# Kernel tuning notes

Hardware: AMD Instinct MI355X
Metric: run time of the kernel (lower is better)

Reference implementation:

```python
import jax, jax.numpy as jnp
import numpy as np
import math

L_S = 64  # segment length (factor)


def setup_inputs() -> dict:
    key = jax.random.key(0)
    kq, kk, kv = jax.random.split(key, 3)
    B, L, H, D = 4, 8192, 16, 64
    return {
        "queries": jax.random.normal(kq, (B, L, H, D), dtype=jnp.float32),
        "keys": jax.random.normal(kk, (B, L, H, D), dtype=jnp.float32),
        "values": jax.random.normal(kv, (B, L, H, D), dtype=jnp.float32),
        "attn_mask": 0,
    }


def reference(queries, keys, values, attn_mask):
    B, L, H, D = queries.shape
    Ls = L_S
    M = L // Ls  # L % Ls == 0 by construction, so addition_Q path is a no-op
    scale = 1.0 / math.sqrt(Ls * D)

    # segment: [B, M, Ls, H, D]
    sq = queries.reshape(B, M, Ls, H, D)
    sk = keys.reshape(B, M, Ls, H, D)
    sv = values.reshape(B, M, Ls, H, D)

    # rfft over head dim D, ortho norm -> [B, M, Ls, H, D//2+1] complex
    qf = jnp.fft.rfft(sq, axis=-1, norm="ortho")
    kf = jnp.fft.rfft(sk, axis=-1, norm="ortho")
    vf = jnp.fft.rfft(sv, axis=-1, norm="ortho")

    # complex segment correlation: [B, H, M, M]
    scores = jnp.einsum("bmlhd,bnlhd->bhmn", qf, jnp.conj(kf)) / math.sqrt(D)
    A = jax.nn.softmax(scale * jnp.abs(scores), axis=-1)  # real
    Ac = A.astype(qf.dtype)  # complex with zero imaginary part

    # complex weighted sum of value spectra: [B, M, Ls, H, D//2+1]
    Vf = jnp.einsum("bhmn,bnlhd->bmlhd", Ac, vf)
    V = jnp.fft.irfft(Vf, n=D, axis=-1, norm="ortho")  # real [B, M, Ls, H, D]
    return V.reshape(B, L, H, D)
```

## Files before the change

### kernel.cpp

```cpp
#include <hip/hip_runtime.h>
#include <cstdint>
#include <cstddef>


typedef short bf16x8 __attribute__((ext_vector_type(8)));
typedef float f32x4 __attribute__((ext_vector_type(4)));

__device__ __forceinline__ ushort f2bf(float f) {
    union { float f; uint32_t u; } v; v.f = f;
    uint32_t r = (v.u + 0x7FFFu + ((v.u >> 16) & 1u)) >> 16;
    return (ushort)r;
}

__global__ void k_gmat(float* __restrict__ GreT, float* __restrict__ GimT) {
    const float lam = 1.0f / 32768.0f;
    const float c = 3.14159265358979323846f / 32.0f;
    for (int e = threadIdx.x + blockIdx.x * blockDim.x; e < 4096; e += blockDim.x * gridDim.x) {
        int dp = e >> 6, d = e & 63;
        int delta = d - dp;
        float re = 0.f, im = 0.f;
        for (int k = 0; k <= 32; ++k) {
            int r = ((k * delta) % 64 + 64) % 64;
            float ang = c * (float)r;
            re += cosf(ang);
            im -= sinf(ang);
        }
        GreT[e] = re * lam;
        GimT[e] = im * lam;
    }
}

__global__ __launch_bounds__(256) void k_prep_q(const float* __restrict__ Q, ushort* __restrict__ Qf) {
    int blk = blockIdx.x;
    int bh = blk >> 7, m = blk & 127;
    int b = bh >> 4, h = bh & 15;
    const float* qbase = Q + ((size_t)(b * 8192 + m * 64)) * 1024 + h * 64;
    ushort* obase = Qf + ((size_t)bh * 128 + m) * 4096;
    for (int idx = threadIdx.x; idx < 1024; idx += 256) {
        int l = idx >> 4, d4 = (idx & 15) * 4;
        float4 v = *(const float4*)(qbase + (size_t)l * 1024 + d4);
        ushort4 o; o.x = f2bf(v.x); o.y = f2bf(v.y); o.z = f2bf(v.z); o.w = f2bf(v.w);
        *(ushort4*)(obase + idx * 4) = o;
    }
}

__global__ __launch_bounds__(256) void k_prep_k(const float* __restrict__ K,
                                                const float* __restrict__ GreT,
                                                const float* __restrict__ GimT,
                                                ushort* __restrict__ Kre, ushort* __restrict__ Kim) {
    __shared__ float gre[4096], gim[4096], kT[4096];
    int blk = blockIdx.x;
    int bh = blk >> 7, n = blk & 127;
    int b = bh >> 4, h = bh & 15;
    int t = threadIdx.x;
    for (int idx = t; idx < 1024; idx += 256) {
        *(float4*)&gre[idx * 4] = *(const float4*)(GreT + idx * 4);
        *(float4*)&gim[idx * 4] = *(const float4*)(GimT + idx * 4);
    }
    int lc = t & 63, dq = t >> 6;
    const float* kbase = K + ((size_t)(b * 8192 + n * 64 + lc)) * 1024 + h * 64;
    #pragma unroll
    for (int r = 0; r < 4; ++r) {
        int d0 = r * 16 + dq * 4;
        float4 v = *(const float4*)(kbase + d0);
        kT[(d0 + 0) * 64 + lc] = v.x; kT[(d0 + 1) * 64 + lc] = v.y;
        kT[(d0 + 2) * 64 + lc] = v.z; kT[(d0 + 3) * 64 + lc] = v.w;
    }
    __syncthreads();
    int d = t & 63, w = t >> 6;
    float re[16], im[16];
    #pragma unroll
    for (int j = 0; j < 16; ++j) { re[j] = 0.f; im[j] = 0.f; }
    for (int dp = 0; dp < 64; ++dp) {
        float gr = gre[dp * 64 + d];
        float gi = gim[dp * 64 + d];
        const float4* kp = (const float4*)&kT[dp * 64 + w * 16];
        #pragma unroll
        for (int q = 0; q < 4; ++q) {
            float4 kv = kp[q];
            re[q * 4 + 0] += gr * kv.x; re[q * 4 + 1] += gr * kv.y;
            re[q * 4 + 2] += gr * kv.z; re[q * 4 + 3] += gr * kv.w;
            im[q * 4 + 0] += gi * kv.x; im[q * 4 + 1] += gi * kv.y;
            im[q * 4 + 2] += gi * kv.z; im[q * 4 + 3] += gi * kv.w;
        }
    }
    ushort* reb = Kre + ((size_t)bh * 128 + n) * 4096;
    ushort* imb = Kim + ((size_t)bh * 128 + n) * 4096;
    #pragma unroll
    for (int j = 0; j < 16; ++j) {
        int off = (w * 16 + j) * 64 + d;
        reb[off] = f2bf(re[j]);
        imb[off] = f2bf(im[j]);
    }
}

__global__ __launch_bounds__(256) void k_scores(const ushort* __restrict__ Qf,
                                                const ushort* __restrict__ Kre,
                                                const ushort* __restrict__ Kim,
                                                float* __restrict__ Sre, float* __restrict__ Sim) {
    __shared__ ushort qt[64 * 72], ret[64 * 72], imt[64 * 72];
    int bh = blockIdx.y;
    int mh = blockIdx.x >> 1, nh = blockIdx.x & 1;
    int m0 = mh * 64, n0 = nh * 64;
    int t = threadIdx.x;
    int lane = t & 63, wave = t >> 6;
    int wm = wave >> 1, wn = wave & 1;
    int row16 = lane & 15, quad = lane >> 4;
    f32x4 accre[2][2] = {};
    f32x4 accim[2][2] = {};
    const ushort* qg = Qf + ((size_t)bh * 128 + m0) * 4096;
    const ushort* rg = Kre + ((size_t)bh * 128 + n0) * 4096;
    const ushort* ig = Kim + ((size_t)bh * 128 + n0) * 4096;
    for (int kt = 0; kt < 64; ++kt) {
        int j0 = kt * 64;
        #pragma unroll
        for (int p = 0; p < 2; ++p) {
            int idx = p * 256 + t;
            int row = idx >> 3, ch = idx & 7;
            size_t go = (size_t)row * 4096 + j0 + ch * 8;
            int lo = row * 72 + ch * 8;
            *(uint4*)&qt[lo]  = *(const uint4*)(qg + go);
            *(uint4*)&ret[lo] = *(const uint4*)(rg + go);
            *(uint4*)&imt[lo] = *(const uint4*)(ig + go);
        }
        __syncthreads();
        #pragma unroll
        for (int kk = 0; kk < 2; ++kk) {
            bf16x8 a[2], br[2], bi[2];
            #pragma unroll
            for (int mt = 0; mt < 2; ++mt)
                a[mt] = *(const bf16x8*)&qt[(wm * 32 + mt * 16 + row16) * 72 + kk * 32 + quad * 8];
            #pragma unroll
            for (int nt = 0; nt < 2; ++nt) {
                br[nt] = *(const bf16x8*)&ret[(wn * 32 + nt * 16 + row16) * 72 + kk * 32 + quad * 8];
                bi[nt] = *(const bf16x8*)&imt[(wn * 32 + nt * 16 + row16) * 72 + kk * 32 + quad * 8];
            }
            #pragma unroll
            for (int mt = 0; mt < 2; ++mt)
                #pragma unroll
                for (int nt = 0; nt < 2; ++nt) {
                    accre[mt][nt] = __builtin_amdgcn_mfma_f32_16x16x32_bf16(a[mt], br[nt], accre[mt][nt], 0, 0, 0);
                    accim[mt][nt] = __builtin_amdgcn_mfma_f32_16x16x32_bf16(a[mt], bi[nt], accim[mt][nt], 0, 0, 0);
                }
        }
        __syncthreads();
    }
    float* sre = Sre + (size_t)bh * 16384;
    float* sim = Sim + (size_t)bh * 16384;
    #pragma unroll
    for (int mt = 0; mt < 2; ++mt)
        #pragma unroll
        for (int nt = 0; nt < 2; ++nt)
            #pragma unroll
            for (int i = 0; i < 4; ++i) {
                int r = m0 + wm * 32 + mt * 16 + quad * 4 + i;
                int c = n0 + wn * 32 + nt * 16 + row16;
                sre[r * 128 + c] = accre[mt][nt][i];
                sim[r * 128 + c] = accim[mt][nt][i];
            }
}

__global__ __launch_bounds__(128) void k_softmax(const float* __restrict__ Sre,
                                                 const float* __restrict__ Sim,
                                                 ushort* __restrict__ A) {
    __shared__ float redmax[2], redsum[2];
    int row = blockIdx.x;
    int t = threadIdx.x;
    size_t off = (size_t)row * 128 + t;
    float re = Sre[off], im = Sim[off];
    float lg = sqrtf(re * re + im * im);
    float v = lg;
    for (int o = 32; o > 0; o >>= 1) v = fmaxf(v, __shfl_xor(v, o));
    if ((t & 63) == 0) redmax[t >> 6] = v;
    __syncthreads();
    float mx = fmaxf(redmax[0], redmax[1]);
    float e = expf(lg - mx);
    float s = e;
    for (int o = 32; o > 0; o >>= 1) s += __shfl_xor(s, o);
    if ((t & 63) == 0) redsum[t >> 6] = s;
    __syncthreads();
    float tot = redsum[0] + redsum[1];
    A[off] = f2bf(e / tot);
}

__global__ __launch_bounds__(256) void k_vt(const float* __restrict__ V, ushort* __restrict__ Vt) {
    __shared__ float tile[64 * 68];
    int l = blockIdx.x, nh = blockIdx.y, bh = blockIdx.z;
    int b = bh >> 4, h = bh & 15;
    int t = threadIdx.x;
    int n = t & 63, dq = t >> 6;
    const float* vbase = V + ((size_t)(b * 8192 + (nh * 64 + n) * 64 + l)) * 1024 + h * 64;
    #pragma unroll
    for (int r = 0; r < 4; ++r) {
        int d0 = r * 16 + dq * 4;
        float4 v = *(const float4*)(vbase + d0);
        tile[(d0 + 0) * 68 + n] = v.x; tile[(d0 + 1) * 68 + n] = v.y;
        tile[(d0 + 2) * 68 + n] = v.z; tile[(d0 + 3) * 68 + n] = v.w;
    }
    __syncthreads();
    int d = t >> 2, cq = t & 3;
    __align__(16) ushort u[16];
    #pragma unroll
    for (int i = 0; i < 16; ++i) u[i] = f2bf(tile[d * 68 + cq * 16 + i]);
    ushort* ob = Vt + ((size_t)bh * 4096 + l * 64 + d) * 128 + nh * 64 + cq * 16;
    *(uint4*)(ob) = *(uint4*)&u[0];
    *(uint4*)(ob + 8) = *(uint4*)&u[8];
}

__global__ __launch_bounds__(256) void k_mix(const ushort* __restrict__ A,
                                             const ushort* __restrict__ Vt,
                                             float* __restrict__ Out) {
    __shared__ ushort At[128 * 136], Vtl[64 * 136];
    int jt = blockIdx.x, bh = blockIdx.y;
    int b = bh >> 4, h = bh & 15;
    int j0 = jt * 64;
    int t = threadIdx.x;
    int lane = t & 63, wave = t >> 6;
    int row16 = lane & 15, quad = lane >> 4;
    const ushort* ag = A + (size_t)bh * 16384;
    const ushort* vg = Vt + ((size_t)bh * 4096 + j0) * 128;
    #pragma unroll
    for (int p = 0; p < 8; ++p) {
        int idx = p * 256 + t;
        int row = idx >> 4, ch = idx & 15;
        *(uint4*)&At[row * 136 + ch * 8] = *(const uint4*)(ag + row * 128 + ch * 8);
    }
    #pragma unroll
    for (int p = 0; p < 4; ++p) {
        int idx = p * 256 + t;
        int row = idx >> 4, ch = idx & 15;
        *(uint4*)&Vtl[row * 136 + ch * 8] = *(const uint4*)(vg + (size_t)row * 128 + ch * 8);
    }
    __syncthreads();
    f32x4 acc[2][4] = {};
    #pragma unroll
    for (int kk = 0; kk < 4; ++kk) {
        bf16x8 a[2], bv[4];
        #pragma unroll
        for (int mt = 0; mt < 2; ++mt)
            a[mt] = *(const bf16x8*)&At[(wave * 32 + mt * 16 + row16) * 136 + kk * 32 + quad * 8];
        #pragma unroll
        for (int j2 = 0; j2 < 4; ++j2)
            bv[j2] = *(const bf16x8*)&Vtl[(j2 * 16 + row16) * 136 + kk * 32 + quad * 8];
        #pragma unroll
        for (int mt = 0; mt < 2; ++mt)
            #pragma unroll
            for (int j2 = 0; j2 < 4; ++j2)
                acc[mt][j2] = __builtin_amdgcn_mfma_f32_16x16x32_bf16(a[mt], bv[j2], acc[mt][j2], 0, 0, 0);
    }
    #pragma unroll
    for (int mt = 0; mt < 2; ++mt)
        #pragma unroll
        for (int j2 = 0; j2 < 4; ++j2)
            #pragma unroll
            for (int i = 0; i < 4; ++i) {
                int m = wave * 32 + mt * 16 + quad * 4 + i;
                int j = j0 + j2 * 16 + row16;
                int ll = j >> 6, d = j & 63;
                Out[((size_t)(b * 8192 + m * 64 + ll)) * 1024 + h * 64 + d] = acc[mt][j2][i];
            }
}

extern "C" void kernel_launch(void* const* d_in, const int* in_sizes, int n_in,
                              void* d_out, int out_size, void* d_ws, size_t ws_size,
                              hipStream_t stream) {
    const float* Q = (const float*)d_in[0];
    const float* K = (const float*)d_in[1];
    const float* V = (const float*)d_in[2];
    float* Out = (float*)d_out;
    char* ws = (char*)d_ws;
    float* GreT = (float*)ws;
    float* GimT = (float*)(ws + 16384);
    float* Sre  = (float*)(ws + 32768);
    float* Sim  = (float*)(ws + 32768 + 4194304);
    ushort* A   = (ushort*)(ws + 32768 + 2 * 4194304);
    ushort* Qf  = (ushort*)(ws + 32768 + 2 * 4194304 + 2097152);
    ushort* Kre = Qf + 33554432;
    ushort* Kim = Kre + 33554432;
    ushort* Vt  = Qf;

    k_gmat<<<16, 256, 0, stream>>>(GreT, GimT);
    k_prep_q<<<8192, 256, 0, stream>>>(Q, Qf);
    k_prep_k<<<8192, 256, 0, stream>>>(K, GreT, GimT, Kre, Kim);
    k_scores<<<dim3(4, 64), 256, 0, stream>>>(Qf, Kre, Kim, Sre, Sim);
    k_softmax<<<8192, 128, 0, stream>>>(Sre, Sim, A);
    k_vt<<<dim3(64, 2, 64), 256, 0, stream>>>(V, Vt);
    k_mix<<<dim3(64, 64), 256, 0, stream>>>(A, Vt, Out);
}
```

Before: 613.8 us.

## Compute K spectral transform with bf16 MFMA using split hi/lo G matrices

The per-segment K transform (a 64x64 matrix times the 64x64 G matrix) moves from scalar fp32 FMAs in shared memory to bf16 MFMA instructions. G is stored as high and low bf16 parts, so two MFMAs per tile keep near-fp32 accuracy in the G operand, while K is rounded to bf16 before the multiply. G fragments are loaded straight from global memory into registers, and shared memory drops from 48KB to about 9KB, which should allow more blocks per CU. The cost is lower precision on the K input and output stores that are scattered by MFMA row layout.

```diff
diff --git a/kernel.cpp b/kernel.cpp
--- a/kernel.cpp
+++ b/kernel.cpp
@@ -12,11 +12,17 @@
     return (ushort)r;
 }
 
-__global__ void k_gmat(float* __restrict__ GreT, float* __restrict__ GimT) {
+__device__ __forceinline__ float bf2f(ushort h) {
+    union { uint32_t u; float f; } v; v.u = ((uint32_t)h) << 16;
+    return v.f;
+}
+
+__global__ void k_gmat(ushort* __restrict__ GreH, ushort* __restrict__ GreL,
+                       ushort* __restrict__ GimH, ushort* __restrict__ GimL) {
     const float lam = 1.0f / 32768.0f;
     const float c = 3.14159265358979323846f / 32.0f;
     for (int e = threadIdx.x + blockIdx.x * blockDim.x; e < 4096; e += blockDim.x * gridDim.x) {
-        int dp = e >> 6, d = e & 63;
+        int d = e >> 6, dp = e & 63;
         int delta = d - dp;
         float re = 0.f, im = 0.f;
         for (int k = 0; k <= 32; ++k) {
@@ -25,8 +31,13 @@
             re += cosf(ang);
             im -= sinf(ang);
         }
-        GreT[e] = re * lam;
-        GimT[e] = im * lam;
+        re *= lam; im *= lam;
+        ushort rh = f2bf(re);
+        GreH[e] = rh;
+        GreL[e] = f2bf(re - bf2f(rh));
+        ushort ih = f2bf(im);
+        GimH[e] = ih;
+        GimL[e] = f2bf(im - bf2f(ih));
     }
 }
 
@@ -45,53 +56,77 @@
 }
 
 __global__ __launch_bounds__(256) void k_prep_k(const float* __restrict__ K,
-                                                const float* __restrict__ GreT,
-                                                const float* __restrict__ GimT,
+                                                const ushort* __restrict__ GreH,
+                                                const ushort* __restrict__ GreL,
+                                                const ushort* __restrict__ GimH,
+                                                const ushort* __restrict__ GimL,
                                                 ushort* __restrict__ Kre, ushort* __restrict__ Kim) {
-    __shared__ float gre[4096], gim[4096], kT[4096];
+    __shared__ ushort kb[64 * 72];
     int blk = blockIdx.x;
     int bh = blk >> 7, n = blk & 127;
     int b = bh >> 4, h = bh & 15;
     int t = threadIdx.x;
-    for (int idx = t; idx < 1024; idx += 256) {
-        *(float4*)&gre[idx * 4] = *(const float4*)(GreT + idx * 4);
-        *(float4*)&gim[idx * 4] = *(const float4*)(GimT + idx * 4);
-    }
-    int lc = t & 63, dq = t >> 6;
-    const float* kbase = K + ((size_t)(b * 8192 + n * 64 + lc)) * 1024 + h * 64;
-    #pragma unroll
-    for (int r = 0; r < 4; ++r) {
-        int d0 = r * 16 + dq * 4;
-        float4 v = *(const float4*)(kbase + d0);
-        kT[(d0 + 0) * 64 + lc] = v.x; kT[(d0 + 1) * 64 + lc] = v.y;
-        kT[(d0 + 2) * 64 + lc] = v.z; kT[(d0 + 3) * 64 + lc] = v.w;
-    }
-    __syncthreads();
-    int d = t & 63, w = t >> 6;
-    float re[16], im[16];
-    #pragma unroll
-    for (int j = 0; j < 16; ++j) { re[j] = 0.f; im[j] = 0.f; }
-    for (int dp = 0; dp < 64; ++dp) {
-        float gr = gre[dp * 64 + d];
-        float gi = gim[dp * 64 + d];
-        const float4* kp = (const float4*)&kT[dp * 64 + w * 16];
-        #pragma unroll
-        for (int q = 0; q < 4; ++q) {
-            float4 kv = kp[q];
-            re[q * 4 + 0] += gr * kv.x; re[q * 4 + 1] += gr * kv.y;
-            re[q * 4 + 2] += gr * kv.z; re[q * 4 + 3] += gr * kv.w;
-            im[q * 4 + 0] += gi * kv.x; im[q * 4 + 1] += gi * kv.y;
-            im[q * 4 + 2] += gi * kv.z; im[q * 4 + 3] += gi * kv.w;
-        }
-    }
+    int lane = t & 63, wave = t >> 6;
+    int wm = wave >> 1, wn = wave & 1;
+    int row16 = lane & 15, quad = lane >> 4;
+
+    bf16x8 grh[2][2], grl[2][2], gih[2][2], gil[2][2];
+    #pragma unroll
+    for (int nt = 0; nt < 2; ++nt)
+        #pragma unroll
+        for (int kk = 0; kk < 2; ++kk) {
+            int off = (wn * 32 + nt * 16 + row16) * 64 + kk * 32 + quad * 8;
+            grh[nt][kk] = *(const bf16x8*)(GreH + off);
+            grl[nt][kk] = *(const bf16x8*)(GreL + off);
+            gih[nt][kk] = *(const bf16x8*)(GimH + off);
+            gil[nt][kk] = *(const bf16x8*)(GimL + off);
+        }
+
+    {
+        int rrow = t >> 2, rcol = (t & 3) * 16;
+        const float* kbase = K + ((size_t)(b * 8192 + n * 64 + rrow)) * 1024 + h * 64 + rcol;
+        ushort* lbase = &kb[rrow * 72 + rcol];
+        #pragma unroll
+        for (int c = 0; c < 4; ++c) {
+            float4 v = *(const float4*)(kbase + c * 4);
+            ushort4 o; o.x = f2bf(v.x); o.y = f2bf(v.y); o.z = f2bf(v.z); o.w = f2bf(v.w);
+            *(ushort4*)(lbase + c * 4) = o;
+        }
+    }
+    __syncthreads();
+
+    f32x4 accre[2][2] = {};
+    f32x4 accim[2][2] = {};
+    #pragma unroll
+    for (int kk = 0; kk < 2; ++kk) {
+        bf16x8 a[2];
+        #pragma unroll
+        for (int mt = 0; mt < 2; ++mt)
+            a[mt] = *(const bf16x8*)&kb[(wm * 32 + mt * 16 + row16) * 72 + kk * 32 + quad * 8];
+        #pragma unroll
+        for (int mt = 0; mt < 2; ++mt)
+            #pragma unroll
+            for (int nt = 0; nt < 2; ++nt) {
+                accre[mt][nt] = __builtin_amdgcn_mfma_f32_16x16x32_bf16(a[mt], grh[nt][kk], accre[mt][nt], 0, 0, 0);
+                accre[mt][nt] = __builtin_amdgcn_mfma_f32_16x16x32_bf16(a[mt], grl[nt][kk], accre[mt][nt], 0, 0, 0);
+                accim[mt][nt] = __builtin_amdgcn_mfma_f32_16x16x32_bf16(a[mt], gih[nt][kk], accim[mt][nt], 0, 0, 0);
+                accim[mt][nt] = __builtin_amdgcn_mfma_f32_16x16x32_bf16(a[mt], gil[nt][kk], accim[mt][nt], 0, 0, 0);
+            }
+    }
+
     ushort* reb = Kre + ((size_t)bh * 128 + n) * 4096;
     ushort* imb = Kim + ((size_t)bh * 128 + n) * 4096;
     #pragma unroll
-    for (int j = 0; j < 16; ++j) {
-        int off = (w * 16 + j) * 64 + d;
-        reb[off] = f2bf(re[j]);
-        imb[off] = f2bf(im[j]);
-    }
+    for (int mt = 0; mt < 2; ++mt)
+        #pragma unroll
+        for (int nt = 0; nt < 2; ++nt)
+            #pragma unroll
+            for (int i = 0; i < 4; ++i) {
+                int l = wm * 32 + mt * 16 + quad * 4 + i;
+                int d = wn * 32 + nt * 16 + row16;
+                reb[l * 64 + d] = f2bf(accre[mt][nt][i]);
+                imb[l * 64 + d] = f2bf(accim[mt][nt][i]);
+            }
 }
 
 __global__ __launch_bounds__(256) void k_scores(const ushort* __restrict__ Qf,
@@ -269,8 +304,10 @@
     const float* V = (const float*)d_in[2];
     float* Out = (float*)d_out;
     char* ws = (char*)d_ws;
-    float* GreT = (float*)ws;
-    float* GimT = (float*)(ws + 16384);
+    ushort* GreH = (ushort*)ws;
+    ushort* GreL = GreH + 4096;
+    ushort* GimH = GreL + 4096;
+    ushort* GimL = GimH + 4096;
     float* Sre  = (float*)(ws + 32768);
     float* Sim  = (float*)(ws + 32768 + 4194304);
     ushort* A   = (ushort*)(ws + 32768 + 2 * 4194304);
@@ -279,9 +316,9 @@
     ushort* Kim = Kre + 33554432;
     ushort* Vt  = Qf;
 
-    k_gmat<<<16, 256, 0, stream>>>(GreT, GimT);
+    k_gmat<<<16, 256, 0, stream>>>(GreH, GreL, GimH, GimL);
     k_prep_q<<<8192, 256, 0, stream>>>(Q, Qf);
-    k_prep_k<<<8192, 256, 0, stream>>>(K, GreT, GimT, Kre, Kim);
+    k_prep_k<<<8192, 256, 0, stream>>>(K, GreH, GreL, GimH, GimL, Kre, Kim);
     k_scores<<<dim3(4, 64), 256, 0, stream>>>(Qf, Kre, Kim, Sre, Sim);
     k_softmax<<<8192, 128, 0, stream>>>(Sre, Sim, A);
     k_vt<<<dim3(64, 2, 64), 256, 0, stream>>>(V, Vt);
```

Measured after the change: 619.4 us. Within noise of the previous version (+0.9%).
